# Optimization experiments

Hardware: AMD Instinct MI355X
Metric: run time of the kernel (lower is better)

## Reference

```python
import jax, jax.numpy as jnp
import numpy as np

N = 50000   # nodes
E = 800000  # edges (avg degree 16)
D = 128     # node latent dim
DE = 128    # edge latent dim
L = 3       # num_mp_steps


def setup_inputs() -> dict:
    key = jax.random.key(0)
    ks = jax.random.split(key, 10)
    s = 0.05
    return dict(
        x=jax.random.normal(ks[0], (N, D), jnp.float32),
        edge_index=jax.random.randint(ks[1], (2, E), 0, N, jnp.int32),
        edge_attr=jax.random.normal(ks[2], (E, DE), jnp.float32),
        # per-layer GATConv params (stacked over L layers)
        W=jax.random.normal(ks[3], (L, D, D), jnp.float32) * s,        # lin (shared src/dst)
        att_src=jax.random.normal(ks[4], (L, D), jnp.float32) * s,
        att_dst=jax.random.normal(ks[5], (L, D), jnp.float32) * s,
        W_e=jax.random.normal(ks[6], (L, DE, D), jnp.float32) * s,     # lin_edge
        att_edge=jax.random.normal(ks[7], (L, D), jnp.float32) * s,
        bias=jnp.zeros((L, D), jnp.float32),
        ln_gamma=jnp.ones((L, D), jnp.float32),                        # post-conv LayerNorm
        ln_beta=jnp.zeros((L, D), jnp.float32),
    )


def reference(x, edge_index, edge_attr, W, att_src, att_dst, W_e, att_edge, bias, ln_gamma, ln_beta):
    n = x.shape[0]
    src, dst = edge_index[0], edge_index[1]

    # add_self_loops with fill_value='mean': self-loop edge feature of node i is
    # the mean of raw edge features of edges incoming to i (0 if none).
    ones = jnp.ones((src.shape[0],), x.dtype)
    deg = jax.ops.segment_sum(ones, dst, num_segments=n)
    loop_attr = jax.ops.segment_sum(edge_attr, dst, num_segments=n) / jnp.maximum(deg, 1.0)[:, None]
    loop = jnp.arange(n, dtype=src.dtype)
    src_f = jnp.concatenate([src, loop])            # [E+N]
    dst_f = jnp.concatenate([dst, loop])            # [E+N]
    ea_f = jnp.concatenate([edge_attr, loop_attr], axis=0)  # [E+N, DE]

    def layer(h_in, p):
        Wl, asl, adl, Wel, ael, bl, gl, bel = p
        h = h_in @ Wl                                              # [N, D]
        # per-edge attention logits (heads=1)
        a = (h @ asl)[src_f] + (h @ adl)[dst_f] + ea_f @ (Wel @ ael)  # [E+N]
        a = jnp.where(a > 0, a, 0.2 * a)                           # LeakyReLU(0.2)
        # segment softmax over destination nodes (every node has a self loop)
        m = jax.ops.segment_max(a, dst_f, num_segments=n)
        ea = jnp.exp(a - m[dst_f])
        denom = jax.ops.segment_sum(ea, dst_f, num_segments=n)
        alpha = ea / denom[dst_f]
        out = jax.ops.segment_sum(h[src_f] * alpha[:, None], dst_f, num_segments=n) + bl
        # LayerNorm (elementwise affine)
        mu = jnp.mean(out, axis=-1, keepdims=True)
        var = jnp.var(out, axis=-1, keepdims=True)
        out = (out - mu) * jax.lax.rsqrt(var + 1e-5) * gl + bel
        return out, None

    h, _ = jax.lax.scan(layer, x, (W, att_src, att_dst, W_e, att_edge, bias, ln_gamma, ln_beta))
    return h
```

## Files before the change

### kernel.cpp

```cpp
#include <hip/hip_runtime.h>
#include <cstdint>

#define D 128
#define LNUM 3

typedef short short8 __attribute__((ext_vector_type(8)));
typedef float f32x4 __attribute__((ext_vector_type(4)));

static __device__ __forceinline__ float wred_sum(float x) {
#pragma unroll
    for (int off = 32; off; off >>= 1) x += __shfl_xor(x, off);
    return x;
}
static __device__ __forceinline__ float wred_max(float x) {
#pragma unroll
    for (int off = 32; off; off >>= 1) x = fmaxf(x, __shfl_xor(x, off));
    return x;
}
static __device__ __forceinline__ uint32_t f2bf_rne(float x) {
    uint32_t u = __float_as_uint(x);
    uint32_t r = u + 0x7fffu + ((u >> 16) & 1u);
    return r >> 16;
}


__global__ __launch_bounds__(256) void pre_k(const float* __restrict__ W, const float* __restrict__ We,
                                             const float* __restrict__ ae, const float* __restrict__ x,
                                             const int* __restrict__ dst,
                                             uint16_t* __restrict__ Wt, float* __restrict__ vbuf,
                                             uint16_t* __restrict__ xb, int* __restrict__ cnt,
                                             int ND4, int E) {
    int tid = blockIdx.x * 256 + threadIdx.x;
    int stride = gridDim.x * 256;
    for (int i = tid; i < ND4; i += stride) {
        float4 v = *(const float4*)&x[(size_t)i * 4];
        uint2 o;
        o.x = f2bf_rne(v.x) | (f2bf_rne(v.y) << 16);
        o.y = f2bf_rne(v.z) | (f2bf_rne(v.w) << 16);
        *(uint2*)&xb[(size_t)i * 4] = o;
    }
    for (int e = tid; e < E; e += stride) atomicAdd(&cnt[dst[e]], 1);
    for (int i = tid; i < LNUM * D * D; i += stride) {
        int l = i >> 14;
        int r = i & (D * D - 1);
        int j = r >> 7, k = r & 127;
        Wt[i] = (uint16_t)f2bf_rne(W[(size_t)l * D * D + (size_t)k * D + j]);
    }
    if (tid < LNUM * D) {
        int l = tid >> 7, j = tid & 127;
        const float* Wrow = We + ((size_t)l * D + j) * D;
        const float* a = ae + (size_t)l * D;
        float s = 0.f;
        for (int d = 0; d < D; ++d) s += Wrow[d] * a[d];
        vbuf[tid] = s;
    }
}


__global__ __launch_bounds__(1024) void scan_k(const int* __restrict__ cnt, int* __restrict__ rowptr, int N) {
    __shared__ int sh[1024];
    int t = threadIdx.x;
    int chunk = (N + 1023) >> 10;
    int b = t * chunk;
    int e = min(b + chunk, N);
    int s = 0;
    for (int i = b; i < e; ++i) s += cnt[i];
    sh[t] = s;
    __syncthreads();
    for (int off = 1; off < 1024; off <<= 1) {
        int v = (t >= off) ? sh[t - off] : 0;
        __syncthreads();
        sh[t] += v;
        __syncthreads();
    }
    int run = sh[t] - s;
    for (int i = b; i < e; ++i) { rowptr[i] = run; run += cnt[i]; }
    if (t == 1023) rowptr[N] = sh[1023];
}


__global__ __launch_bounds__(256) void fillec_k(const float* __restrict__ ea, const float* __restrict__ vbuf,
                                                const int* __restrict__ src, const int* __restrict__ dst,
                                                const int* __restrict__ rowptr, int* __restrict__ cnt,
                                                uint4* __restrict__ rec, int E) {
    int t = threadIdx.x;
    int sub = t & 7;
    float4 vr[3][4];
#pragma unroll
    for (int l = 0; l < 3; ++l)
#pragma unroll
        for (int i = 0; i < 4; ++i)
            vr[l][i] = *(const float4*)&vbuf[l * D + sub * 16 + i * 4];

    for (int e0 = blockIdx.x * 32; e0 < E; e0 += gridDim.x * 32) {
        int e = e0 + (t >> 3);
        if (e >= E) continue;
        const float* row = ea + (size_t)e * D + sub * 16;
        float p0 = 0.f, p1 = 0.f, p2 = 0.f;
#pragma unroll
        for (int i = 0; i < 4; ++i) {
            float4 v = *(const float4*)&row[i * 4];
            p0 += v.x * vr[0][i].x + v.y * vr[0][i].y + v.z * vr[0][i].z + v.w * vr[0][i].w;
            p1 += v.x * vr[1][i].x + v.y * vr[1][i].y + v.z * vr[1][i].z + v.w * vr[1][i].w;
            p2 += v.x * vr[2][i].x + v.y * vr[2][i].y + v.z * vr[2][i].z + v.w * vr[2][i].w;
        }
#pragma unroll
        for (int off = 1; off < 8; off <<= 1) {
            p0 += __shfl_xor(p0, off);
            p1 += __shfl_xor(p1, off);
            p2 += __shfl_xor(p2, off);
        }
        if (sub == 0) {
            int d = dst[e];
            int p = atomicSub(&cnt[d], 1) - 1;
            int q = rowptr[d] + p;
            uint4 r;
            r.x = (uint32_t)src[e];
            r.y = __float_as_uint(p0);
            r.z = __float_as_uint(p1);
            r.w = __float_as_uint(p2);
            rec[q] = r;
        }
    }
}


__global__ __launch_bounds__(256) void gemm_mfma_k(const uint16_t* __restrict__ A,
                                                   const uint16_t* __restrict__ Wt,
                                                   const float* __restrict__ as_,
                                                   const float* __restrict__ ad_,
                                                   uint16_t* __restrict__ hbf,
                                                   float* __restrict__ hs, float* __restrict__ hd, int N) {
    __shared__ uint4 As[64 * 16];
    int t = threadIdx.x;
    int row0 = blockIdx.x * 64;
#pragma unroll
    for (int it = 0; it < 4; ++it) {
        int idx2 = it * 256 + t;
        int r = idx2 >> 4, s = idx2 & 15;
        int gr = row0 + r;
        uint4 v = make_uint4(0u, 0u, 0u, 0u);
        if (gr < N) v = *(const uint4*)&A[(size_t)gr * D + s * 8];
        As[r * 16 + (s ^ (r & 7))] = v;
    }
    __syncthreads();
    int w = t >> 6, l = t & 63;
    int lrow = l & 15, lk = l >> 4;
    int rbase = w * 16;
    short8 afrag[4];
#pragma unroll
    for (int ks = 0; ks < 4; ++ks) {
        int r = rbase + lrow;
        int s = (ks * 4 + lk) ^ (r & 7);
        afrag[ks] = __builtin_bit_cast(short8, As[r * 16 + s]);
    }
    float psum[4] = {0.f, 0.f, 0.f, 0.f}, pdum[4] = {0.f, 0.f, 0.f, 0.f};
#pragma unroll
    for (int ct = 0; ct < 8; ++ct) {
        f32x4 acc = {0.f, 0.f, 0.f, 0.f};
#pragma unroll
        for (int ks = 0; ks < 4; ++ks) {
            short8 b = *(const short8*)&Wt[(size_t)(ct * 16 + lrow) * D + ks * 32 + lk * 8];
            acc = __builtin_amdgcn_mfma_f32_16x16x32_bf16(afrag[ks], b, acc, 0, 0, 0);
        }
        int col_g = ct * 16 + lrow;
        float av = as_[col_g], dv = ad_[col_g];
#pragma unroll
        for (int r = 0; r < 4; ++r) {
            float v = acc[r];
            psum[r] += v * av;
            pdum[r] += v * dv;
            int row_g = row0 + rbase + lk * 4 + r;
            if (row_g < N) hbf[(size_t)row_g * D + col_g] = (uint16_t)f2bf_rne(v);
        }
    }
#pragma unroll
    for (int r = 0; r < 4; ++r) {
        float ps = psum[r], pd = pdum[r];
#pragma unroll
        for (int off = 1; off < 16; off <<= 1) {
            ps += __shfl_xor(ps, off);
            pd += __shfl_xor(pd, off);
        }
        if (lrow == 0) {
            int row_g = row0 + rbase + lk * 4 + r;
            if (row_g < N) { hs[row_g] = ps; hd[row_g] = pd; }
        }
    }
}


__global__ __launch_bounds__(256) void node_k(const uint32_t* __restrict__ hb, const float* __restrict__ hs,
                                              const float* __restrict__ hd, const uint4* __restrict__ rec,
                                              const int* __restrict__ rowptr,
                                              const float* __restrict__ bias, const float* __restrict__ gamma,
                                              const float* __restrict__ beta,
                                              uint32_t* __restrict__ outb, float* __restrict__ outf,
                                              int N, int lsel) {
    __shared__ float s_al[4][66];
    __shared__ int s_co[4][66];
    int w = threadIdx.x >> 6;
    int lane = threadIdx.x & 63;
    int wid = blockIdx.x * 4 + w;
    if (wid >= N) return;
    int beg = rowptr[wid], end = rowptr[wid + 1];
    int deg = end - beg;
    float hdi = hd[wid];
    float hsi = hs[wid];
    float acc0 = 0.f, acc1 = 0.f;

    if (deg <= 63) {
        int ne = deg + 1;
        bool v = lane < deg;
        uint4 r = v ? rec[beg + lane] : make_uint4(0u, 0u, 0u, 0u);
        int col = (int)r.x;
        uint32_t ecu = lsel == 0 ? r.y : (lsel == 1 ? r.z : r.w);
        float ec = __uint_as_float(ecu);
        float hsc = v ? hs[col] : 0.f;
        s_co[w][lane] = col;
        if (lane == 0) { s_co[w][deg] = wid; }
        __asm__ volatile("s_waitcnt lgkmcnt(0)" ::: "memory");

        uint32_t rb[4][8];
        bool fast = ne <= 32;
        if (fast) {
#pragma unroll
            for (int g = 0; g < 4; ++g) {
                if (g * 8 < ne) {
#pragma unroll
                    for (int j0 = 0; j0 < 8; ++j0) {
                        int c = s_co[w][g * 8 + j0];
                        rb[g][j0] = hb[(size_t)c * 64 + lane];
                    }
                }
            }
        }

        float a = v ? (hsc + hdi + ec) : -3e38f;
        a = a > 0.f ? a : 0.2f * a;
        float sumec = wred_sum(v ? ec : 0.f);
        float ecs = deg > 0 ? sumec / (float)deg : 0.f;
        float as_ = hsi + hdi + ecs;
        as_ = as_ > 0.f ? as_ : 0.2f * as_;
        float m = fmaxf(wred_max(a), as_);
        float p = __expf(a - m);
        float ps = __expf(as_ - m);
        float denom = wred_sum(p) + ps;
        float inv = 1.f / denom;
        s_al[w][lane] = p * inv;
        if (lane == 0) { s_al[w][deg] = ps * inv; }
        __asm__ volatile("s_waitcnt lgkmcnt(0)" ::: "memory");

        if (fast) {
#pragma unroll
            for (int g = 0; g < 4; ++g) {
                if (g * 8 < ne) {
#pragma unroll
                    for (int j0 = 0; j0 < 8; ++j0) {
                        float al = s_al[w][g * 8 + j0];
                        uint32_t b = rb[g][j0];
                        acc0 += al * __uint_as_float(b << 16);
                        acc1 += al * __uint_as_float(b & 0xffff0000u);
                    }
                }
            }
        } else {
            int j = 0;
            for (; j + 4 <= ne; j += 4) {
                int c0 = s_co[w][j], c1 = s_co[w][j + 1], c2 = s_co[w][j + 2], c3 = s_co[w][j + 3];
                float a0 = s_al[w][j], a1 = s_al[w][j + 1], a2 = s_al[w][j + 2], a3 = s_al[w][j + 3];
                uint32_t b0 = hb[(size_t)c0 * 64 + lane];
                uint32_t b1 = hb[(size_t)c1 * 64 + lane];
                uint32_t b2 = hb[(size_t)c2 * 64 + lane];
                uint32_t b3 = hb[(size_t)c3 * 64 + lane];
                acc0 += a0 * __uint_as_float(b0 << 16) + a1 * __uint_as_float(b1 << 16) +
                        a2 * __uint_as_float(b2 << 16) + a3 * __uint_as_float(b3 << 16);
                acc1 += a0 * __uint_as_float(b0 & 0xffff0000u) + a1 * __uint_as_float(b1 & 0xffff0000u) +
                        a2 * __uint_as_float(b2 & 0xffff0000u) + a3 * __uint_as_float(b3 & 0xffff0000u);
            }
            for (; j < ne; ++j) {
                int c0 = s_co[w][j];
                float a0 = s_al[w][j];
                uint32_t b0 = hb[(size_t)c0 * 64 + lane];
                acc0 += a0 * __uint_as_float(b0 << 16);
                acc1 += a0 * __uint_as_float(b0 & 0xffff0000u);
            }
        }
    } else {
        float m = -3e38f, dsum = 0.f, sumec = 0.f;
        for (int base = 0; base < deg; base += 64) {
            int jj = base + lane;
            bool v = jj < deg;
            uint4 r = v ? rec[beg + jj] : make_uint4(0u, 0u, 0u, 0u);
            uint32_t ecu = lsel == 0 ? r.y : (lsel == 1 ? r.z : r.w);
            float ec = __uint_as_float(ecu);
            float a = v ? (hs[(int)r.x] + hdi + ec) : -3e38f;
            a = a > 0.f ? a : 0.2f * a;
            sumec += wred_sum(v ? ec : 0.f);
            float cm = wred_max(a);
            float nm = fmaxf(m, cm);
            dsum = dsum * __expf(m - nm) + wred_sum(__expf(a - nm));
            m = nm;
        }
        float ecs = sumec / (float)deg;
        float as_ = hsi + hdi + ecs;
        as_ = as_ > 0.f ? as_ : 0.2f * as_;
        float nm = fmaxf(m, as_);
        dsum = dsum * __expf(m - nm) + __expf(as_ - nm);
        m = nm;
        float inv = 1.f / dsum;
        for (int base = 0; base < deg; base += 64) {
            int jj = base + lane;
            bool v = jj < deg;
            uint4 r = v ? rec[beg + jj] : make_uint4(0u, 0u, 0u, 0u);
            int col = (int)r.x;
            uint32_t ecu = lsel == 0 ? r.y : (lsel == 1 ? r.z : r.w);
            float ec = __uint_as_float(ecu);
            float a = v ? (hs[col] + hdi + ec) : -3e38f;
            a = a > 0.f ? a : 0.2f * a;
            __asm__ volatile("s_waitcnt lgkmcnt(0)" ::: "memory");
            s_al[w][lane] = __expf(a - m) * inv;
            s_co[w][lane] = col;
            __asm__ volatile("s_waitcnt lgkmcnt(0)" ::: "memory");
            int cnt = min(64, deg - base);
            for (int k = 0; k < cnt; ++k) {
                int c = s_co[w][k];
                float al = s_al[w][k];
                uint32_t b = hb[(size_t)c * 64 + lane];
                acc0 += al * __uint_as_float(b << 16);
                acc1 += al * __uint_as_float(b & 0xffff0000u);
            }
        }
        float alS = __expf(as_ - m) * inv;
        uint32_t b = hb[(size_t)wid * 64 + lane];
        acc0 += alS * __uint_as_float(b << 16);
        acc1 += alS * __uint_as_float(b & 0xffff0000u);
    }

    float2 bi = *(const float2*)&bias[lane * 2];
    float o0 = acc0 + bi.x, o1 = acc1 + bi.y;
    float mean = wred_sum(o0 + o1) * (1.f / 128.f);
    float d0 = o0 - mean, d1 = o1 - mean;
    float var = wred_sum(d0 * d0 + d1 * d1) * (1.f / 128.f);
    float rstd = rsqrtf(var + 1e-5f);
    float2 g = *(const float2*)&gamma[lane * 2];
    float2 be = *(const float2*)&beta[lane * 2];
    float2 o;
    o.x = d0 * rstd * g.x + be.x;
    o.y = d1 * rstd * g.y + be.y;
    if (outf) {
        *(float2*)&outf[(size_t)wid * D + lane * 2] = o;
    } else {
        outb[(size_t)wid * 64 + lane] = f2bf_rne(o.x) | (f2bf_rne(o.y) << 16);
    }
}


extern "C" void kernel_launch(void* const* d_in, const int* in_sizes, int n_in,
                              void* d_out, int out_size, void* d_ws, size_t ws_size,
                              hipStream_t stream) {
    const float* x = (const float*)d_in[0];
    const int* ei = (const int*)d_in[1];
    const float* ea = (const float*)d_in[2];
    const float* W = (const float*)d_in[3];
    const float* att_src = (const float*)d_in[4];
    const float* att_dst = (const float*)d_in[5];
    const float* We = (const float*)d_in[6];
    const float* att_edge = (const float*)d_in[7];
    const float* bias = (const float*)d_in[8];
    const float* gamma = (const float*)d_in[9];
    const float* beta = (const float*)d_in[10];

    int N = in_sizes[0] / D;
    int E = in_sizes[1] / 2;
    const int* srcA = ei;
    const int* dstA = ei + E;

    float* p = (float*)d_ws;
    float* hsb = p;   p += N;
    float* hdb = p;   p += N;
    float* vbuf = p;  p += LNUM * D + 128;
    uint16_t* xb = (uint16_t*)p;
    uint16_t* hbf = xb + (size_t)N * D;
    uint16_t* hnb = hbf + (size_t)N * D;
    uint16_t* Wt = hnb + (size_t)N * D;
    uint4* rec = (uint4*)(Wt + (size_t)LNUM * D * D);
    int* ip = (int*)(rec + E);
    int* rowptr = ip; ip += N + 1;
    int* cnt = ip;    ip += N;

    hipMemsetAsync(cnt, 0, sizeof(int) * N, stream);
    pre_k<<<1536, 256, 0, stream>>>(W, We, att_edge, x, dstA, Wt, vbuf, xb, cnt, N * D / 4, E);
    scan_k<<<1, 1024, 0, stream>>>(cnt, rowptr, N);
    fillec_k<<<(E + 31) / 32, 256, 0, stream>>>(ea, vbuf, srcA, dstA, rowptr, cnt, rec, E);

    const uint16_t* hin = xb;
    for (int l = 0; l < LNUM; ++l) {
        gemm_mfma_k<<<(N + 63) / 64, 256, 0, stream>>>(hin, Wt + (size_t)l * D * D,
                                                       att_src + (size_t)l * D, att_dst + (size_t)l * D,
                                                       hbf, hsb, hdb, N);
        bool last = (l == LNUM - 1);
        node_k<<<(N + 3) / 4, 256, 0, stream>>>((const uint32_t*)hbf, hsb, hdb, rec, rowptr,
                                                bias + (size_t)l * D, gamma + (size_t)l * D,
                                                beta + (size_t)l * D,
                                                last ? nullptr : (uint32_t*)hnb,
                                                last ? (float*)d_out : nullptr, N, l);
        hin = hnb;
    }
}
```

Before: 438.8 us.

## Fuse layer-0 GEMM with edge-record fill kernel and vectorize aggregation accumulators

Result: faster. 417.3 us (-4.9%).

```diff
diff --git a/kernel.cpp b/kernel.cpp
--- a/kernel.cpp
+++ b/kernel.cpp
@@ -6,6 +6,7 @@
 
 typedef short short8 __attribute__((ext_vector_type(8)));
 typedef float f32x4 __attribute__((ext_vector_type(4)));
+typedef float f32x2 __attribute__((ext_vector_type(2)));
 
 static __device__ __forceinline__ float wred_sum(float x) {
 #pragma unroll
@@ -79,11 +80,86 @@
 }
 
 
-__global__ __launch_bounds__(256) void fillec_k(const float* __restrict__ ea, const float* __restrict__ vbuf,
-                                                const int* __restrict__ src, const int* __restrict__ dst,
-                                                const int* __restrict__ rowptr, int* __restrict__ cnt,
-                                                uint4* __restrict__ rec, int E) {
+static __device__ __forceinline__ void gemm_body(uint4* As, int bid, int t,
+                                                 const uint16_t* __restrict__ A,
+                                                 const uint16_t* __restrict__ Wt,
+                                                 const float* __restrict__ as_,
+                                                 const float* __restrict__ ad_,
+                                                 uint16_t* __restrict__ hbf,
+                                                 float* __restrict__ hs, float* __restrict__ hd, int N) {
+    int row0 = bid * 64;
+#pragma unroll
+    for (int it = 0; it < 4; ++it) {
+        int idx2 = it * 256 + t;
+        int r = idx2 >> 4, s = idx2 & 15;
+        int gr = row0 + r;
+        uint4 v = make_uint4(0u, 0u, 0u, 0u);
+        if (gr < N) v = *(const uint4*)&A[(size_t)gr * D + s * 8];
+        As[r * 16 + (s ^ (r & 7))] = v;
+    }
+    __syncthreads();
+    int w = t >> 6, l = t & 63;
+    int lrow = l & 15, lk = l >> 4;
+    int rbase = w * 16;
+    short8 afrag[4];
+#pragma unroll
+    for (int ks = 0; ks < 4; ++ks) {
+        int r = rbase + lrow;
+        int s = (ks * 4 + lk) ^ (r & 7);
+        afrag[ks] = __builtin_bit_cast(short8, As[r * 16 + s]);
+    }
+    float psum[4] = {0.f, 0.f, 0.f, 0.f}, pdum[4] = {0.f, 0.f, 0.f, 0.f};
+#pragma unroll
+    for (int ct = 0; ct < 8; ++ct) {
+        f32x4 acc = {0.f, 0.f, 0.f, 0.f};
+#pragma unroll
+        for (int ks = 0; ks < 4; ++ks) {
+            short8 b = *(const short8*)&Wt[(size_t)(ct * 16 + lrow) * D + ks * 32 + lk * 8];
+            acc = __builtin_amdgcn_mfma_f32_16x16x32_bf16(afrag[ks], b, acc, 0, 0, 0);
+        }
+        int col_g = ct * 16 + lrow;
+        float av = as_[col_g], dv = ad_[col_g];
+#pragma unroll
+        for (int r = 0; r < 4; ++r) {
+            float v = acc[r];
+            psum[r] += v * av;
+            pdum[r] += v * dv;
+            int row_g = row0 + rbase + lk * 4 + r;
+            if (row_g < N) hbf[(size_t)row_g * D + col_g] = (uint16_t)f2bf_rne(v);
+        }
+    }
+#pragma unroll
+    for (int r = 0; r < 4; ++r) {
+        float ps = psum[r], pd = pdum[r];
+#pragma unroll
+        for (int off = 1; off < 16; off <<= 1) {
+            ps += __shfl_xor(ps, off);
+            pd += __shfl_xor(pd, off);
+        }
+        if (lrow == 0) {
+            int row_g = row0 + rbase + lk * 4 + r;
+            if (row_g < N) { hs[row_g] = ps; hd[row_g] = pd; }
+        }
+    }
+}
+
+
+__global__ __launch_bounds__(256) void fg_k(const uint16_t* __restrict__ A, const uint16_t* __restrict__ Wt,
+                                            const float* __restrict__ as_, const float* __restrict__ ad_,
+                                            uint16_t* __restrict__ hbf, float* __restrict__ hs,
+                                            float* __restrict__ hd, int N,
+                                            const float* __restrict__ ea, const float* __restrict__ vbuf,
+                                            const int* __restrict__ src, const int* __restrict__ dst,
+                                            const int* __restrict__ rowptr, int* __restrict__ cnt,
+                                            uint4* __restrict__ rec, int E, int NB_G) {
+    __shared__ uint4 As[64 * 16];
     int t = threadIdx.x;
+    if ((int)blockIdx.x < NB_G) {
+        gemm_body(As, blockIdx.x, t, A, Wt, as_, ad_, hbf, hs, hd, N);
+        return;
+    }
+    int bid = blockIdx.x - NB_G;
+    int nbF = gridDim.x - NB_G;
     int sub = t & 7;
     float4 vr[3][4];
 #pragma unroll
@@ -92,7 +168,7 @@
         for (int i = 0; i < 4; ++i)
             vr[l][i] = *(const float4*)&vbuf[l * D + sub * 16 + i * 4];
 
-    for (int e0 = blockIdx.x * 32; e0 < E; e0 += gridDim.x * 32) {
+    for (int e0 = bid * 32; e0 < E; e0 += nbF * 32) {
         int e = e0 + (t >> 3);
         if (e >= E) continue;
         const float* row = ea + (size_t)e * D + sub * 16;
@@ -132,61 +208,7 @@
                                                    uint16_t* __restrict__ hbf,
                                                    float* __restrict__ hs, float* __restrict__ hd, int N) {
     __shared__ uint4 As[64 * 16];
-    int t = threadIdx.x;
-    int row0 = blockIdx.x * 64;
-#pragma unroll
-    for (int it = 0; it < 4; ++it) {
-        int idx2 = it * 256 + t;
-        int r = idx2 >> 4, s = idx2 & 15;
-        int gr = row0 + r;
-        uint4 v = make_uint4(0u, 0u, 0u, 0u);
-        if (gr < N) v = *(const uint4*)&A[(size_t)gr * D + s * 8];
-        As[r * 16 + (s ^ (r & 7))] = v;
-    }
-    __syncthreads();
-    int w = t >> 6, l = t & 63;
-    int lrow = l & 15, lk = l >> 4;
-    int rbase = w * 16;
-    short8 afrag[4];
-#pragma unroll
-    for (int ks = 0; ks < 4; ++ks) {
-        int r = rbase + lrow;
-        int s = (ks * 4 + lk) ^ (r & 7);
-        afrag[ks] = __builtin_bit_cast(short8, As[r * 16 + s]);
-    }
-    float psum[4] = {0.f, 0.f, 0.f, 0.f}, pdum[4] = {0.f, 0.f, 0.f, 0.f};
-#pragma unroll
-    for (int ct = 0; ct < 8; ++ct) {
-        f32x4 acc = {0.f, 0.f, 0.f, 0.f};
-#pragma unroll
-        for (int ks = 0; ks < 4; ++ks) {
-            short8 b = *(const short8*)&Wt[(size_t)(ct * 16 + lrow) * D + ks * 32 + lk * 8];
-            acc = __builtin_amdgcn_mfma_f32_16x16x32_bf16(afrag[ks], b, acc, 0, 0, 0);
-        }
-        int col_g = ct * 16 + lrow;
-        float av = as_[col_g], dv = ad_[col_g];
-#pragma unroll
-        for (int r = 0; r < 4; ++r) {
-            float v = acc[r];
-            psum[r] += v * av;
-            pdum[r] += v * dv;
-            int row_g = row0 + rbase + lk * 4 + r;
-            if (row_g < N) hbf[(size_t)row_g * D + col_g] = (uint16_t)f2bf_rne(v);
-        }
-    }
-#pragma unroll
-    for (int r = 0; r < 4; ++r) {
-        float ps = psum[r], pd = pdum[r];
-#pragma unroll
-        for (int off = 1; off < 16; off <<= 1) {
-            ps += __shfl_xor(ps, off);
-            pd += __shfl_xor(pd, off);
-        }
-        if (lrow == 0) {
-            int row_g = row0 + rbase + lk * 4 + r;
-            if (row_g < N) { hs[row_g] = ps; hd[row_g] = pd; }
-        }
-    }
+    gemm_body(As, blockIdx.x, threadIdx.x, A, Wt, as_, ad_, hbf, hs, hd, N);
 }
 
 
@@ -207,7 +229,7 @@
     int deg = end - beg;
     float hdi = hd[wid];
     float hsi = hs[wid];
-    float acc0 = 0.f, acc1 = 0.f;
+    f32x2 acc2 = {0.f, 0.f};
 
     if (deg <= 63) {
         int ne = deg + 1;
@@ -259,8 +281,10 @@
                     for (int j0 = 0; j0 < 8; ++j0) {
                         float al = s_al[w][g * 8 + j0];
                         uint32_t b = rb[g][j0];
-                        acc0 += al * __uint_as_float(b << 16);
-                        acc1 += al * __uint_as_float(b & 0xffff0000u);
+                        f32x2 hv;
+                        hv.x = __uint_as_float(b << 16);
+                        hv.y = __uint_as_float(b & 0xffff0000u);
+                        acc2 += hv * al;
                     }
                 }
             }
@@ -273,17 +297,18 @@
                 uint32_t b1 = hb[(size_t)c1 * 64 + lane];
                 uint32_t b2 = hb[(size_t)c2 * 64 + lane];
                 uint32_t b3 = hb[(size_t)c3 * 64 + lane];
-                acc0 += a0 * __uint_as_float(b0 << 16) + a1 * __uint_as_float(b1 << 16) +
-                        a2 * __uint_as_float(b2 << 16) + a3 * __uint_as_float(b3 << 16);
-                acc1 += a0 * __uint_as_float(b0 & 0xffff0000u) + a1 * __uint_as_float(b1 & 0xffff0000u) +
-                        a2 * __uint_as_float(b2 & 0xffff0000u) + a3 * __uint_as_float(b3 & 0xffff0000u);
+                f32x2 h0; h0.x = __uint_as_float(b0 << 16); h0.y = __uint_as_float(b0 & 0xffff0000u);
+                f32x2 h1; h1.x = __uint_as_float(b1 << 16); h1.y = __uint_as_float(b1 & 0xffff0000u);
+                f32x2 h2; h2.x = __uint_as_float(b2 << 16); h2.y = __uint_as_float(b2 & 0xffff0000u);
+                f32x2 h3; h3.x = __uint_as_float(b3 << 16); h3.y = __uint_as_float(b3 & 0xffff0000u);
+                acc2 += h0 * a0 + h1 * a1 + h2 * a2 + h3 * a3;
             }
             for (; j < ne; ++j) {
                 int c0 = s_co[w][j];
                 float a0 = s_al[w][j];
                 uint32_t b0 = hb[(size_t)c0 * 64 + lane];
-                acc0 += a0 * __uint_as_float(b0 << 16);
-                acc1 += a0 * __uint_as_float(b0 & 0xffff0000u);
+                f32x2 h0; h0.x = __uint_as_float(b0 << 16); h0.y = __uint_as_float(b0 & 0xffff0000u);
+                acc2 += h0 * a0;
             }
         }
     } else {
@@ -327,18 +352,18 @@
                 int c = s_co[w][k];
                 float al = s_al[w][k];
                 uint32_t b = hb[(size_t)c * 64 + lane];
-                acc0 += al * __uint_as_float(b << 16);
-                acc1 += al * __uint_as_float(b & 0xffff0000u);
+                f32x2 h0; h0.x = __uint_as_float(b << 16); h0.y = __uint_as_float(b & 0xffff0000u);
+                acc2 += h0 * al;
             }
         }
         float alS = __expf(as_ - m) * inv;
         uint32_t b = hb[(size_t)wid * 64 + lane];
-        acc0 += alS * __uint_as_float(b << 16);
-        acc1 += alS * __uint_as_float(b & 0xffff0000u);
+        f32x2 hS; hS.x = __uint_as_float(b << 16); hS.y = __uint_as_float(b & 0xffff0000u);
+        acc2 += hS * alS;
     }
 
     float2 bi = *(const float2*)&bias[lane * 2];
-    float o0 = acc0 + bi.x, o1 = acc1 + bi.y;
+    float o0 = acc2.x + bi.x, o1 = acc2.y + bi.y;
     float mean = wred_sum(o0 + o1) * (1.f / 128.f);
     float d0 = o0 - mean, d1 = o1 - mean;
     float var = wred_sum(d0 * d0 + d1 * d1) * (1.f / 128.f);
@@ -392,10 +417,16 @@
     hipMemsetAsync(cnt, 0, sizeof(int) * N, stream);
     pre_k<<<1536, 256, 0, stream>>>(W, We, att_edge, x, dstA, Wt, vbuf, xb, cnt, N * D / 4, E);
     scan_k<<<1, 1024, 0, stream>>>(cnt, rowptr, N);
-    fillec_k<<<(E + 31) / 32, 256, 0, stream>>>(ea, vbuf, srcA, dstA, rowptr, cnt, rec, E);
-
-    const uint16_t* hin = xb;
-    for (int l = 0; l < LNUM; ++l) {
+
+    int NB_G = (N + 63) / 64;
+    int NB_F = (E + 31) / 32;
+    fg_k<<<NB_G + NB_F, 256, 0, stream>>>(xb, Wt, att_src, att_dst, hbf, hsb, hdb, N,
+                                          ea, vbuf, srcA, dstA, rowptr, cnt, rec, E, NB_G);
+    node_k<<<(N + 3) / 4, 256, 0, stream>>>((const uint32_t*)hbf, hsb, hdb, rec, rowptr,
+                                            bias, gamma, beta, (uint32_t*)hnb, nullptr, N, 0);
+
+    const uint16_t* hin = hnb;
+    for (int l = 1; l < LNUM; ++l) {
         gemm_mfma_k<<<(N + 63) / 64, 256, 0, stream>>>(hin, Wt + (size_t)l * D * D,
                                                        att_src + (size_t)l * D, att_dst + (size_t)l * D,
                                                        hbf, hsb, hdb, N);
```
